# Performance work log

Hardware: AMD Instinct MI355X
Metric: run time of the kernel (lower is better)

The kernel has to match this reference:

```python
import jax, jax.numpy as jnp
import numpy as np

B, S, D = 1, 2048, 512
H, KH, DH = 8, 2, 64
G = H // KH            # grouped queries per kv head
CBS = SBS = 32         # compress / selection block size (equal)
NSEL = 8               # num selected blocks
WIN = 128              # sliding window size
NC = S // CBS          # num compressed blocks
NF = S // SBS          # num fine blocks (S divisible by SBS)
CDIM = CBS * DH


def setup_inputs():
    key = jax.random.key(0)
    ks = jax.random.split(key, 12)
    r = lambda k, shape, s=0.02: jax.random.normal(k, shape, dtype=jnp.float32) * s
    return {
        "inp": jax.random.normal(ks[0], (B, S, D), dtype=jnp.float32),
        "norm_w": jnp.ones((D,), jnp.float32),
        "w_qkv": r(ks[1], (D, H * DH + 2 * KH * DH)),
        "mem_kv": r(ks[2], (2, KH, 1, DH)),
        "k_pos": r(ks[3], (KH, CBS, DH)),
        "v_pos": r(ks[4], (KH, CBS, DH)),
        "kc_w1": r(ks[5], (CDIM, CDIM)), "kc_b1": jnp.zeros((CDIM,), jnp.float32),
        "kc_w2": r(ks[6], (CDIM, DH)), "kc_b2": jnp.zeros((DH,), jnp.float32),
        "vc_w1": r(ks[7], (CDIM, CDIM)), "vc_b1": jnp.zeros((CDIM,), jnp.float32),
        "vc_w2": r(ks[8], (CDIM, DH)), "vc_b2": jnp.zeros((DH,), jnp.float32),
        "comb_w": r(ks[9], (D, 3 * H)),
        "comb_b": jnp.tile(jnp.array([-2.0, -2.0, 2.0], jnp.float32), H),
        "out_w": r(ks[10], (H * DH, D)),
    }


def _rope(x):  # x: [b, h, n, d]; interleaved rotary (rotary-embedding-torch style)
    d, n = x.shape[-1], x.shape[-2]
    inv = 1.0 / (10000.0 ** (jnp.arange(0, d, 2, dtype=jnp.float32) / d))
    fr = jnp.arange(n, dtype=jnp.float32)[:, None] * inv[None, :]  # [n, d/2]
    fr = jnp.repeat(fr, 2, axis=-1)                                 # [n, d]
    cos, sin = jnp.cos(fr), jnp.sin(fr)
    xp = x.reshape(*x.shape[:-1], d // 2, 2)
    xr = jnp.stack((-xp[..., 1], xp[..., 0]), axis=-1).reshape(x.shape)
    return x * cos + xr * sin


def _mlp(x, w1, b1, w2, b2):
    return jax.nn.relu(x @ w1 + b1) @ w2 + b2


def _forward(inp, norm_w, w_qkv, mem_kv, k_pos, v_pos, kc_w1, kc_b1, kc_w2, kc_b2,
             vc_w1, vc_b1, vc_w2, vc_b2, comb_w, comb_b, out_w):
    scale = DH ** -0.5
    NEG = -jnp.finfo(jnp.float32).max

    # RMSNorm
    x = inp * jax.lax.rsqrt(jnp.mean(inp * inp, -1, keepdims=True)
                            + jnp.finfo(jnp.float32).eps) * norm_w

    qkv = x @ w_qkv
    q, k, v = jnp.split(qkv, [H * DH, H * DH + KH * DH], axis=-1)
    q = q.reshape(B, S, H, DH).transpose(0, 2, 1, 3)    # b h n d
    k = k.reshape(B, S, KH, DH).transpose(0, 2, 1, 3)   # b kh n d
    v = v.reshape(B, S, KH, DH).transpose(0, 2, 1, 3)

    # --- 1. compressed attention (unrotated q/k) ---
    kb = k.reshape(B, KH, NC, CBS, DH) + k_pos[None, :, None]
    vb = v.reshape(B, KH, NC, CBS, DH) + v_pos[None, :, None]
    ck = _mlp(kb.reshape(B, KH, NC, CDIM), kc_w1, kc_b1, kc_w2, kc_b2)  # b kh nc d
    cv = _mlp(vb.reshape(B, KH, NC, CDIM), vc_w1, vc_b1, vc_w2, vc_b2)
    ck = jnp.concatenate((jnp.broadcast_to(mem_kv[0][None], (B, KH, 1, DH)), ck), axis=2)
    cv = jnp.concatenate((jnp.broadcast_to(mem_kv[1][None], (B, KH, 1, DH)), cv), axis=2)

    ck_pos = jnp.concatenate((jnp.array([-1]), (jnp.arange(NC) + 1) * CBS - 1))
    cmask = ck_pos[None, :] < jnp.arange(S)[:, None]     # [S, 1+NC]

    qg = q.reshape(B, KH, G, S, DH)
    csim = jnp.einsum('bhgid,bhjd->bhgij', qg, ck) * scale
    csim = jnp.where(cmask, csim, NEG)
    cattn = jax.nn.softmax(csim, axis=-1)
    c_out = jnp.einsum('bhgij,bhjd->bhgid', cattn, cv)   # b kh g n d

    # --- importance scores -> top-k block selection (shared across grouped queries) ---
    imp = csim[..., 1:].mean(axis=2)                     # b kh n nc
    imp = jnp.pad(imp, ((0, 0), (0, 0), (0, 0), (1, 0)), constant_values=-1e3)
    imp = jax.nn.softmax(imp, axis=-1)[..., 1:]
    sel_val, sel_idx = jax.lax.top_k(imp, NSEL)          # b kh n sel

    # --- rotary for fine + sliding branches ---
    qr, kr = _rope(q), _rope(k)

    # --- 2. fine (selected-block) attention ---
    own = jnp.broadcast_to((jnp.arange(S) // SBS)[None, None, :, None], (B, KH, S, 1))
    sel_idx = jnp.concatenate((sel_idx, own), axis=-1)   # b kh n (sel+1), own block appended

    bmask = jnp.broadcast_to((sel_val > 1e-10)[..., None], (B, KH, S, NSEL, SBS))
    tri = jnp.tril(jnp.ones((SBS, SBS), bool))
    diag = jnp.broadcast_to(jnp.tile(tri, (NF, 1))[None, None, :, None, :], (B, KH, S, 1, SBS))
    fmask = jnp.concatenate((bmask, diag), axis=-2).reshape(B, KH, 1, S, (NSEL + 1) * SBS)

    kfb = kr.reshape(B, KH, NF, SBS, DH)
    vfb = v.reshape(B, KH, NF, SBS, DH)
    gidx = sel_idx[..., None, None]                      # b kh n sel1 1 1
    fk = jnp.take_along_axis(kfb[:, :, None], gidx, axis=3).reshape(B, KH, S, (NSEL + 1) * SBS, DH)
    fv = jnp.take_along_axis(vfb[:, :, None], gidx, axis=3).reshape(B, KH, S, (NSEL + 1) * SBS, DH)

    fqg = qr.reshape(B, KH, G, S, DH)
    fsim = jnp.einsum('bhgid,bhijd->bhgij', fqg, fk) * scale
    fsim = jnp.where(fmask, fsim, NEG)
    fattn = jax.nn.softmax(fsim, axis=-1)
    f_out = jnp.einsum('bhgij,bhijd->bhgid', fattn, fv)  # b kh g n d

    diff = jnp.arange(S)[:, None] - jnp.arange(S)[None, :]
    smask = (diff >= 0) & (diff <= WIN)
    ssim = jnp.einsum('bhgid,bhjd->bhgij', fqg, kr) * scale
    ssim = jnp.where(smask, ssim, NEG)
    sattn = jax.nn.softmax(ssim, axis=-1)
    s_out = jnp.einsum('bhgij,bhjd->bhgid', sattn, v)    # b kh g n d

    # --- learned gating combine over [compressed, fine, sliding] ---
    gates = jax.nn.sigmoid(x @ comb_w + comb_b).reshape(B, S, H, 3)
    gates = gates.transpose(0, 2, 1, 3).reshape(B, KH, G, S, 3)
    out = gates[..., 0:1] * c_out + gates[..., 1:2] * f_out + gates[..., 2:3] * s_out
    out = out.reshape(B, H, S, DH).transpose(0, 2, 1, 3).reshape(B, S, H * DH)
    return out @ out_w


def reference(inp, norm_w, w_qkv, mem_kv, k_pos, v_pos, kc_w1, kc_b1, kc_w2, kc_b2,
              vc_w1, vc_b1, vc_w2, vc_b2, comb_w, comb_b, out_w):
    return _forward(inp, norm_w, w_qkv, mem_kv, k_pos, v_pos, kc_w1, kc_b1, kc_w2, kc_b2,
                    vc_w1, vc_b1, vc_w2, vc_b2, comb_w, comb_b, out_w)
```

## Files before the change

### kernel.cpp

```cpp
#include <hip/hip_runtime.h>
#include <hip/hip_bf16.h>
#include <math.h>

#define S 2048
#define D 512
#define H 8
#define KH 2
#define DH 64
#define G 4
#define CBS 32
#define NSEL 8
#define WIN 128
#define NC 64
#define CDIM 2048

typedef __attribute__((ext_vector_type(8))) short bf16x8_t;
typedef __attribute__((ext_vector_type(4))) float f32x4_t;
typedef __attribute__((ext_vector_type(2))) _Float16 half2v;

static __device__ __forceinline__ unsigned short f2bf(float f) {
    union { float f; unsigned int u; } v; v.f = f;
    unsigned int r = (v.u + 0x7FFFu + ((v.u >> 16) & 1u)) >> 16;
    return (unsigned short)r;
}
static __device__ __forceinline__ float bf2f(unsigned short h) {
    union { unsigned int u; float f; } v; v.u = ((unsigned int)h) << 16;
    return v.f;
}
static __device__ __forceinline__ float bflo(unsigned int u) {
    union { unsigned int u; float f; } v; v.u = u << 16; return v.f;
}
static __device__ __forceinline__ float bfhi(unsigned int u) {
    union { unsigned int u; float f; } v; v.u = u & 0xffff0000u; return v.f;
}
static __device__ __forceinline__ unsigned short f2h(float f) {
    union { _Float16 h; unsigned short s; } v; v.h = (_Float16)f; return v.s;
}
static __device__ __forceinline__ float h2f(unsigned short u) {
    union { unsigned short s; _Float16 h; } v; v.s = u; return (float)v.h;
}
static __device__ __forceinline__ float dot2f16(unsigned int a, unsigned int b, float c) {
    union { unsigned int u; half2v h; } A, B; A.u = a; B.u = b;
    return __builtin_amdgcn_fdot2(A.h, B.h, c, false);
}

__global__ __launch_bounds__(256) void k_rmsnorm(const float* __restrict__ inp,
                                                 const float* __restrict__ w,
                                                 unsigned short* __restrict__ xbf) {
    int s = blockIdx.x; int t = threadIdx.x;
    const float* row = inp + (size_t)s * D;
    float a = row[t], b = row[t + 256];
    float ss = a * a + b * b;
    for (int off = 32; off; off >>= 1) ss += __shfl_xor(ss, off);
    __shared__ float red[4];
    if ((t & 63) == 0) red[t >> 6] = ss;
    __syncthreads();
    float tot = red[0] + red[1] + red[2] + red[3];
    float inv = rsqrtf(tot / (float)D + 1.1920929e-07f);
    xbf[(size_t)s * D + t]       = f2bf(a * inv * w[t]);
    xbf[(size_t)s * D + t + 256] = f2bf(b * inv * w[t + 256]);
}

__global__ void k_rope_table(float* __restrict__ ct, float* __restrict__ st) {
    int idx = blockIdx.x * 256 + threadIdx.x;
    int s = idx >> 5, p = idx & 31;
    float inv = powf(10000.0f, -(float)p / 32.0f);
    float fr = (float)s * inv;
    ct[idx] = cosf(fr); st[idx] = sinf(fr);
}

__global__ __launch_bounds__(256) void k_gemm0(
    const unsigned short* __restrict__ A,
    const float* __restrict__ W,
    const float* __restrict__ k_pos, const float* __restrict__ v_pos,
    const float* __restrict__ ct, const float* __restrict__ st,
    float* __restrict__ qb,
    unsigned short* __restrict__ qr16, unsigned short* __restrict__ kr16,
    unsigned short* __restrict__ v16, unsigned short* __restrict__ kbvb)
{
    const int K = 512, N = 768;
    __shared__ __align__(16) unsigned short As[64][40];
    __shared__ __align__(16) unsigned short Bs[64][40];
    int t = threadIdx.x;
    int m0 = blockIdx.y * 64, n0 = blockIdx.x * 64;
    int wave = t >> 6, lane = t & 63;
    int mh = wave & 1, nh = wave >> 1;
    f32x4_t acc[2][2] = {};
    int ar = t >> 2, ac = (t & 3) * 8;
    int bk = t >> 3, bn = (t & 7) * 8;
    int arow_l = lane & 15, kcol = (lane >> 4) * 8;
    uint4 aReg = *(const uint4*)&A[(size_t)(m0 + ar) * K + ac];
    const float4* wr = (const float4*)&W[(size_t)bk * N + n0 + bn];
    float4 w0 = wr[0], w1 = wr[1];
    for (int k0 = 0; k0 < K; k0 += 32) {
        __syncthreads();
        *(uint4*)&As[ar][ac] = aReg;
        unsigned short bp[8];
        bp[0] = f2bf(w0.x); bp[1] = f2bf(w0.y); bp[2] = f2bf(w0.z); bp[3] = f2bf(w0.w);
        bp[4] = f2bf(w1.x); bp[5] = f2bf(w1.y); bp[6] = f2bf(w1.z); bp[7] = f2bf(w1.w);
        #pragma unroll
        for (int j = 0; j < 8; ++j) Bs[bn + j][bk] = bp[j];
        __syncthreads();
        if (k0 + 32 < K) {
            aReg = *(const uint4*)&A[(size_t)(m0 + ar) * K + k0 + 32 + ac];
            wr = (const float4*)&W[(size_t)(k0 + 32 + bk) * N + n0 + bn];
            w0 = wr[0]; w1 = wr[1];
        }
        bf16x8_t a0 = *(const bf16x8_t*)&As[mh * 32 + arow_l][kcol];
        bf16x8_t a1 = *(const bf16x8_t*)&As[mh * 32 + 16 + arow_l][kcol];
        bf16x8_t b0v = *(const bf16x8_t*)&Bs[nh * 32 + arow_l][kcol];
        bf16x8_t b1v = *(const bf16x8_t*)&Bs[nh * 32 + 16 + arow_l][kcol];
        acc[0][0] = __builtin_amdgcn_mfma_f32_16x16x32_bf16(a0, b0v, acc[0][0], 0, 0, 0);
        acc[0][1] = __builtin_amdgcn_mfma_f32_16x16x32_bf16(a0, b1v, acc[0][1], 0, 0, 0);
        acc[1][0] = __builtin_amdgcn_mfma_f32_16x16x32_bf16(a1, b0v, acc[1][0], 0, 0, 0);
        acc[1][1] = __builtin_amdgcn_mfma_f32_16x16x32_bf16(a1, b1v, acc[1][1], 0, 0, 0);
    }
    #pragma unroll
    for (int mi = 0; mi < 2; ++mi)
    #pragma unroll
    for (int ni = 0; ni < 2; ++ni)
    #pragma unroll
    for (int r = 0; r < 4; ++r) {
        int gm = m0 + mh * 32 + mi * 16 + (lane >> 4) * 4 + r;
        int gn = n0 + nh * 32 + ni * 16 + (lane & 15);
        float val = acc[mi][ni][r];
        float part = __shfl_xor(val, 1);
        if (gn < 512) {
            int hh = gn >> 6, d = gn & 63;
            size_t idx = ((size_t)hh * S + gm) * DH + d;
            qb[idx] = val;
            int p = d >> 1;
            float cc = ct[gm * 32 + p], sn = st[gm * 32 + p];
            float y = (d & 1) ? (val * cc + part * sn) : (val * cc - part * sn);
            qr16[idx] = f2h(y);
        } else if (gn < 640) {
            int gk = gn - 512, khh = gk >> 6, d = gk & 63;
            size_t idx = ((size_t)khh * S + gm) * DH + d;
            int p = d >> 1;
            float cc = ct[gm * 32 + p], sn = st[gm * 32 + p];
            float y = (d & 1) ? (val * cc + part * sn) : (val * cc - part * sn);
            kr16[idx] = f2h(y);
            int tt = gm & 31, nc2 = gm >> 5;
            kbvb[((size_t)(khh * 64 + nc2)) * 2048 + tt * 64 + d] =
                f2bf(val + k_pos[(khh * CBS + tt) * 64 + d]);
        } else {
            int gv = gn - 640, khh = gv >> 6, d = gv & 63;
            size_t idx = ((size_t)khh * S + gm) * DH + d;
            v16[idx] = f2bf(val);
            int tt = gm & 31, nc2 = gm >> 5;
            kbvb[((size_t)(128 + khh * 64 + nc2)) * 2048 + tt * 64 + d] =
                f2bf(val + v_pos[(khh * CBS + tt) * 64 + d]);
        }
    }
}

template<int MODE>
__global__ __launch_bounds__(256) void k_gemm(
    const unsigned short* __restrict__ A,
    const float* __restrict__ B0,
    int M, int N, int K,
    float* __restrict__ outC)
{
    __shared__ __align__(16) unsigned short As[64][40];
    __shared__ __align__(16) unsigned short Bs[64][40];
    int t = threadIdx.x;
    int m0 = blockIdx.y * 64, n0 = blockIdx.x * 64;
    const float* W = B0;
    int wave = t >> 6, lane = t & 63;
    int mh = wave & 1, nh = wave >> 1;
    f32x4_t acc[2][2] = {};
    int ar = t >> 2, ac = (t & 3) * 8;
    int bk = t >> 3, bn = (t & 7) * 8;
    int arow_l = lane & 15, kcol = (lane >> 4) * 8;
    uint4 aReg = *(const uint4*)&A[(size_t)(m0 + ar) * K + ac];
    const float4* wr = (const float4*)&W[(size_t)bk * N + n0 + bn];
    float4 w0 = wr[0], w1 = wr[1];
    for (int k0 = 0; k0 < K; k0 += 32) {
        __syncthreads();
        *(uint4*)&As[ar][ac] = aReg;
        unsigned short bp[8];
        bp[0] = f2bf(w0.x); bp[1] = f2bf(w0.y); bp[2] = f2bf(w0.z); bp[3] = f2bf(w0.w);
        bp[4] = f2bf(w1.x); bp[5] = f2bf(w1.y); bp[6] = f2bf(w1.z); bp[7] = f2bf(w1.w);
        #pragma unroll
        for (int j = 0; j < 8; ++j) Bs[bn + j][bk] = bp[j];
        __syncthreads();
        if (k0 + 32 < K) {
            aReg = *(const uint4*)&A[(size_t)(m0 + ar) * K + k0 + 32 + ac];
            wr = (const float4*)&W[(size_t)(k0 + 32 + bk) * N + n0 + bn];
            w0 = wr[0]; w1 = wr[1];
        }
        bf16x8_t a0 = *(const bf16x8_t*)&As[mh * 32 + arow_l][kcol];
        bf16x8_t a1 = *(const bf16x8_t*)&As[mh * 32 + 16 + arow_l][kcol];
        bf16x8_t b0v = *(const bf16x8_t*)&Bs[nh * 32 + arow_l][kcol];
        bf16x8_t b1v = *(const bf16x8_t*)&Bs[nh * 32 + 16 + arow_l][kcol];
        acc[0][0] = __builtin_amdgcn_mfma_f32_16x16x32_bf16(a0, b0v, acc[0][0], 0, 0, 0);
        acc[0][1] = __builtin_amdgcn_mfma_f32_16x16x32_bf16(a0, b1v, acc[0][1], 0, 0, 0);
        acc[1][0] = __builtin_amdgcn_mfma_f32_16x16x32_bf16(a1, b0v, acc[1][0], 0, 0, 0);
        acc[1][1] = __builtin_amdgcn_mfma_f32_16x16x32_bf16(a1, b1v, acc[1][1], 0, 0, 0);
    }
    #pragma unroll
    for (int mi = 0; mi < 2; ++mi)
    #pragma unroll
    for (int ni = 0; ni < 2; ++ni)
    #pragma unroll
    for (int r = 0; r < 4; ++r) {
        int gm = m0 + mh * 32 + mi * 16 + (lane >> 4) * 4 + r;
        int gn = n0 + nh * 32 + ni * 16 + (lane & 15);
        outC[(size_t)gm * N + gn] = acc[mi][ni][r];
    }
}

__global__ __launch_bounds__(256) void k_gemm1p(
    const unsigned short* __restrict__ A,
    const float* __restrict__ kc_w1, const float* __restrict__ vc_w1,
    float* __restrict__ part)
{
    const int N = 2048, LDA = 2048;
    __shared__ __align__(16) unsigned short As[64][40];
    __shared__ __align__(16) unsigned short Bs[64][40];
    int t = threadIdx.x;
    int mb = blockIdx.y & 3, ks = blockIdx.y >> 2;
    int m0 = mb * 64, n0 = blockIdx.x * 64, kbeg = ks * 1024;
    const float* W = (mb >= 2) ? vc_w1 : kc_w1;
    int wave = t >> 6, lane = t & 63;
    int mh = wave & 1, nh = wave >> 1;
    f32x4_t acc[2][2] = {};
    int ar = t >> 2, ac = (t & 3) * 8;
    int bk = t >> 3, bn = (t & 7) * 8;
    int arow_l = lane & 15, kcol = (lane >> 4) * 8;
    uint4 aReg = *(const uint4*)&A[(size_t)(m0 + ar) * LDA + kbeg + ac];
    const float4* wr = (const float4*)&W[(size_t)(kbeg + bk) * N + n0 + bn];
    float4 w0 = wr[0], w1 = wr[1];
    for (int k0 = 0; k0 < 1024; k0 += 32) {
        __syncthreads();
        *(uint4*)&As[ar][ac] = aReg;
        unsigned short bp[8];
        bp[0] = f2bf(w0.x); bp[1] = f2bf(w0.y); bp[2] = f2bf(w0.z); bp[3] = f2bf(w0.w);
        bp[4] = f2bf(w1.x); bp[5] = f2bf(w1.y); bp[6] = f2bf(w1.z); bp[7] = f2bf(w1.w);
        #pragma unroll
        for (int j = 0; j < 8; ++j) Bs[bn + j][bk] = bp[j];
        __syncthreads();
        if (k0 + 32 < 1024) {
            aReg = *(const uint4*)&A[(size_t)(m0 + ar) * LDA + kbeg + k0 + 32 + ac];
            wr = (const float4*)&W[(size_t)(kbeg + k0 + 32 + bk) * N + n0 + bn];
            w0 = wr[0]; w1 = wr[1];
        }
        bf16x8_t a0 = *(const bf16x8_t*)&As[mh * 32 + arow_l][kcol];
        bf16x8_t a1 = *(const bf16x8_t*)&As[mh * 32 + 16 + arow_l][kcol];
        bf16x8_t b0v = *(const bf16x8_t*)&Bs[nh * 32 + arow_l][kcol];
        bf16x8_t b1v = *(const bf16x8_t*)&Bs[nh * 32 + 16 + arow_l][kcol];
        acc[0][0] = __builtin_amdgcn_mfma_f32_16x16x32_bf16(a0, b0v, acc[0][0], 0, 0, 0);
        acc[0][1] = __builtin_amdgcn_mfma_f32_16x16x32_bf16(a0, b1v, acc[0][1], 0, 0, 0);
        acc[1][0] = __builtin_amdgcn_mfma_f32_16x16x32_bf16(a1, b0v, acc[1][0], 0, 0, 0);
        acc[1][1] = __builtin_amdgcn_mfma_f32_16x16x32_bf16(a1, b1v, acc[1][1], 0, 0, 0);
    }
    #pragma unroll
    for (int mi = 0; mi < 2; ++mi)
    #pragma unroll
    for (int ni = 0; ni < 2; ++ni)
    #pragma unroll
    for (int r = 0; r < 4; ++r) {
        int gm = m0 + mh * 32 + mi * 16 + (lane >> 4) * 4 + r;
        int gn = n0 + nh * 32 + ni * 16 + (lane & 15);
        part[((size_t)ks * 256 + gm) * N + gn] = acc[mi][ni][r];
    }
}

__global__ __launch_bounds__(256) void k_gemm1r(
    const float4* __restrict__ part, const float* __restrict__ kc_b1,
    const float* __restrict__ vc_b1, uint2* __restrict__ hid)
{
    int idx = blockIdx.x * 256 + threadIdx.x;
    int gm = idx >> 9, gn4 = (idx & 511) * 4;
    float4 a = part[idx], b = part[idx + 131072];
    const float* bias = (gm >= 128) ? vc_b1 : kc_b1;
    float r0 = fmaxf(a.x + b.x + bias[gn4 + 0], 0.f);
    float r1 = fmaxf(a.y + b.y + bias[gn4 + 1], 0.f);
    float r2 = fmaxf(a.z + b.z + bias[gn4 + 2], 0.f);
    float r3 = fmaxf(a.w + b.w + bias[gn4 + 3], 0.f);
    uint2 o;
    o.x = (unsigned)f2bf(r0) | ((unsigned)f2bf(r1) << 16);
    o.y = (unsigned)f2bf(r2) | ((unsigned)f2bf(r3) << 16);
    hid[idx] = o;
}

__global__ __launch_bounds__(256) void k_mlp2p(
    const unsigned short* __restrict__ A,
    const float* __restrict__ kc_w2, const float* __restrict__ vc_w2,
    float* __restrict__ part)
{
    const int N = 64, LDA = 2048;
    __shared__ __align__(16) unsigned short As[64][40];
    __shared__ __align__(16) unsigned short Bs[64][40];
    int t = threadIdx.x;
    int ks = blockIdx.x, m0 = blockIdx.y * 64;
    int kbeg = ks * 512;
    const float* W = (blockIdx.y >= 2) ? vc_w2 : kc_w2;
    int wave = t >> 6, lane = t & 63;
    int mh = wave & 1, nh = wave >> 1;
    f32x4_t acc[2][2] = {};
    int ar = t >> 2, ac = (t & 3) * 8;
    int bk = t >> 3, bn = (t & 7) * 8;
    int arow_l = lane & 15, kcol = (lane >> 4) * 8;
    uint4 aReg = *(const uint4*)&A[(size_t)(m0 + ar) * LDA + kbeg + ac];
    const float4* wr = (const float4*)&W[(size_t)(kbeg + bk) * N + bn];
    float4 w0 = wr[0], w1 = wr[1];
    for (int k0 = 0; k0 < 512; k0 += 32) {
        __syncthreads();
        *(uint4*)&As[ar][ac] = aReg;
        unsigned short bp[8];
        bp[0] = f2bf(w0.x); bp[1] = f2bf(w0.y); bp[2] = f2bf(w0.z); bp[3] = f2bf(w0.w);
        bp[4] = f2bf(w1.x); bp[5] = f2bf(w1.y); bp[6] = f2bf(w1.z); bp[7] = f2bf(w1.w);
        #pragma unroll
        for (int j = 0; j < 8; ++j) Bs[bn + j][bk] = bp[j];
        __syncthreads();
        if (k0 + 32 < 512) {
            aReg = *(const uint4*)&A[(size_t)(m0 + ar) * LDA + kbeg + k0 + 32 + ac];
            wr = (const float4*)&W[(size_t)(kbeg + k0 + 32 + bk) * N + bn];
            w0 = wr[0]; w1 = wr[1];
        }
        bf16x8_t a0 = *(const bf16x8_t*)&As[mh * 32 + arow_l][kcol];
        bf16x8_t a1 = *(const bf16x8_t*)&As[mh * 32 + 16 + arow_l][kcol];
        bf16x8_t b0v = *(const bf16x8_t*)&Bs[nh * 32 + arow_l][kcol];
        bf16x8_t b1v = *(const bf16x8_t*)&Bs[nh * 32 + 16 + arow_l][kcol];
        acc[0][0] = __builtin_amdgcn_mfma_f32_16x16x32_bf16(a0, b0v, acc[0][0], 0, 0, 0);
        acc[0][1] = __builtin_amdgcn_mfma_f32_16x16x32_bf16(a0, b1v, acc[0][1], 0, 0, 0);
        acc[1][0] = __builtin_amdgcn_mfma_f32_16x16x32_bf16(a1, b0v, acc[1][0], 0, 0, 0);
        acc[1][1] = __builtin_amdgcn_mfma_f32_16x16x32_bf16(a1, b1v, acc[1][1], 0, 0, 0);
    }
    #pragma unroll
    for (int mi = 0; mi < 2; ++mi)
    #pragma unroll
    for (int ni = 0; ni < 2; ++ni)
    #pragma unroll
    for (int r = 0; r < 4; ++r) {
        int gm = m0 + mh * 32 + mi * 16 + (lane >> 4) * 4 + r;
        int gn = nh * 32 + ni * 16 + (lane & 15);
        part[((size_t)ks * 256 + gm) * 64 + gn] = acc[mi][ni][r];
    }
}

__global__ __launch_bounds__(256) void k_mlp2r(
    const float* __restrict__ part, const float* __restrict__ kc_b2,
    const float* __restrict__ vc_b2, const float* __restrict__ mem_kv,
    float* __restrict__ ck, float* __restrict__ cv)
{
    int idx = blockIdx.x * 256 + threadIdx.x;
    int gm = idx >> 6, gn = idx & 63;
    float sum = part[(size_t)gm * 64 + gn] + part[(size_t)(256 + gm) * 64 + gn]
              + part[(size_t)(512 + gm) * 64 + gn] + part[(size_t)(768 + gm) * 64 + gn];
    bool isv = gm >= 128;
    sum += isv ? vc_b2[gn] : kc_b2[gn];
    float* dst = isv ? cv : ck;
    int kh2 = (gm >> 6) & 1, nc2 = gm & 63;
    dst[(kh2 * 65 + 1 + nc2) * 64 + gn] = sum;
    if (blockIdx.x == 0 && threadIdx.x < 256) {
        int t = threadIdx.x;
        int path2 = t >> 7, khm = (t >> 6) & 1, dm = t & 63;
        float* dstm = path2 ? cv : ck;
        dstm[khm * 65 * 64 + dm] = mem_kv[path2 * (KH * DH) + khm * DH + dm];
    }
}

__global__ __launch_bounds__(256) void k_cattn(
    const float* __restrict__ q, const float* __restrict__ ck, const float* __restrict__ cv,
    float* __restrict__ c_out, int* __restrict__ sel)
{
    int kh = blockIdx.x >> 9, sc = blockIdx.x & 511;
    int s_base = sc * 4;
    __shared__ float ckT[64][65];
    __shared__ float cvL[64][66];
    __shared__ float qL[4][64];
    __shared__ float simL[4][64];
    __shared__ float pL[4][64];
    int t = threadIdx.x;
    for (int idx = t; idx < 4096; idx += 256) {
        int j = idx >> 6, d = idx & 63;
        ckT[d][j] = ck[(kh * 65 + j) * 64 + d];
        cvL[j][d] = cv[(kh * 65 + j) * 64 + d];
    }
    int g = t >> 6, lane = t & 63;
    for (int si = 0; si < 4; ++si) {
        int s = s_base + si;
        __syncthreads();
        qL[g][lane] = q[((kh * G + g) * S + s) * DH + lane];
        __syncthreads();
        int j = lane;
        bool valid = (j == 0) || (s >= j * 32);
        float sim = 0.f;
        #pragma unroll 8
        for (int d = 0; d < 64; ++d) sim += qL[g][d] * ckT[d][j];
        sim *= 0.125f;
        float simm = valid ? sim : -INFINITY;
        simL[g][j] = simm;
        float m = simm;
        for (int off = 32; off; off >>= 1) m = fmaxf(m, __shfl_xor(m, off));
        float p = valid ? __expf(simm - m) : 0.f;
        float den = p;
        for (int off = 32; off; off >>= 1) den += __shfl_xor(den, off);
        pL[g][j] = p / den;
        float acc = 0.f;
        #pragma unroll
        for (int j4 = 0; j4 < 16; ++j4) {
            float4 p4 = *(const float4*)&pL[g][j4 * 4];
            acc += p4.x * cvL[j4 * 4 + 0][lane] + p4.y * cvL[j4 * 4 + 1][lane]
                 + p4.z * cvL[j4 * 4 + 2][lane] + p4.w * cvL[j4 * 4 + 3][lane];
        }
        c_out[((kh * G + g) * S + s) * DH + lane] = acc;
        __syncthreads();
        if (g == 0) {
            int l = lane;
            float lv = -INFINITY;
            if (l < 63 && s >= (l + 1) * 32)
                lv = 0.25f * (simL[0][l + 1] + simL[1][l + 1] + simL[2][l + 1] + simL[3][l + 1]);
            float mm = lv;
            for (int off = 32; off; off >>= 1) mm = fmaxf(mm, __shfl_xor(mm, off));
            mm = fmaxf(mm, -1000.0f);
            float e = (lv == -INFINITY) ? 0.f : __expf(lv - mm);
            float dd = e;
            for (int off = 32; off; off >>= 1) dd += __shfl_xor(dd, off);
            dd += __expf(-1000.0f - mm);
            float val = e / dd;
            float vc = val;
            int base = (kh * S + s) * 9;
            for (int t8 = 0; t8 < 8; ++t8) {
                float bv2 = vc; int bi = l;
                for (int off = 32; off; off >>= 1) {
                    float ov = __shfl_xor(bv2, off); int oi = __shfl_xor(bi, off);
                    if (ov > bv2 || (ov == bv2 && oi < bi)) { bv2 = ov; bi = oi; }
                }
                if (l == 0) sel[base + t8] = (bv2 > 1e-10f) ? bi : -1;
                if (l == bi) vc = -1.f;
            }
            if (l == 0) sel[base + 8] = s >> 5;
        }
    }
}

__global__ __launch_bounds__(256, 4) void k_swattn(
    const unsigned short* __restrict__ qr16, const unsigned short* __restrict__ kr16,
    const unsigned short* __restrict__ v16, const int* __restrict__ sel,
    float* __restrict__ fob, float* __restrict__ sob)
{
    int kh = blockIdx.x >> 11, s = blockIdx.x & 2047;
    int t = threadIdx.x, w = t >> 6, lane = t & 63, g = w;
    __shared__ __align__(16) unsigned char KL[64 * 128];
    __shared__ __align__(16) unsigned char VL[64 * 144];
    __shared__ unsigned short qL16[4][64];
    __shared__ float pL[4][64];

    qL16[g][lane] = qr16[(((size_t)kh * G + g) * S + s) * DH + lane];

    int base = (kh * S + s) * 9;
    int lo = s - WIN; if (lo < 0) lo = 0;

    int nv = 0;
    #pragma unroll
    for (int i = 0; i < 8; ++i) nv += (sel[base + i] >= 0) ? 1 : 0;
    int npairF = (nv + 1) >> 1;
    int nchS = (s - lo + 63) >> 6;
    int nch = npairF + nchS;
    int ownStart = s & ~31;
    bool hasOwn = (s & 31) != 0;

    float lF = 0.f, lS = 0.f;
    float a0F = 0.f, a1F = 0.f, a0S = 0.f, a1S = 0.f;
    int h = lane >> 5, dhalf = lane & 31;
    int key = w * 16 + (lane & 15);
    int grpA = lane >> 4;
    uint4 z = make_uint4(0, 0, 0, 0);
    uint4 kd0 = z, kd1 = z, vd0 = z, vd1 = z;

    auto issue = [&](int c) {
        int gkey; bool kv;
        if (c < npairF) {
            int b = sel[base + 2 * c + ((key >> 5) & 1)];
            kv = b >= 0;
            gkey = (kv ? b : 0) * 32 + (key & 31);
        } else {
            gkey = lo + (c - npairF) * 64 + key;
            kv = gkey < s;
        }
        const uint4* kp = (const uint4*)&kr16[((size_t)kh * S + gkey) * DH];
        const uint4* vp = (const uint4*)&v16 [((size_t)kh * S + gkey) * DH];
        kd0 = kv ? kp[grpA] : z;
        kd1 = kv ? kp[grpA + 4] : z;
        vd0 = kv ? vp[grpA] : z;
        vd1 = kv ? vp[grpA + 4] : z;
    };

    issue(0);
    for (int c = 0; c < nch; ++c) {
        __syncthreads();
        *(uint4*)(KL + key * 128 + 16 * (grpA ^ (key & 7))) = kd0;
        *(uint4*)(KL + key * 128 + 16 * ((grpA + 4) ^ (key & 7))) = kd1;
        *(uint4*)(VL + key * 144 + 16 * grpA) = vd0;
        *(uint4*)(VL + key * 144 + 16 * (grpA + 4)) = vd1;
        __syncthreads();
        if (c + 1 < nch) issue(c + 1);

        int j = lane;
        bool isPair = c < npairF;
        int cs = c - npairF;
        int gk0 = lo + cs * 64;
        bool valid = isPair ? ((j < 32) || ((2 * c + 1) < nv))
                            : ((gk0 + j) < s);

        float sva = 0.f, svb = 0.f, svc = 0.f, svd = 0.f;
        #pragma unroll
        for (int grp = 0; grp < 8; ++grp) {
            uint4 kk = *(const uint4*)(KL + j * 128 + 16 * (grp ^ (j & 7)));
            uint4 qq = *(const uint4*)((const unsigned char*)qL16 + g * 128 + 16 * grp);
            sva = dot2f16(kk.x, qq.x, sva);
            svb = dot2f16(kk.y, qq.y, svb);
            svc = dot2f16(kk.z, qq.z, svc);
            svd = dot2f16(kk.w, qq.w, svd);
        }
        float sv = (sva + svb) + (svc + svd);
        float p = valid ? __expf(sv * 0.125f) : 0.f;
        pL[g][j] = p;

        bool doOwn = (!isPair) && hasOwn && (cs == nchS - 1);
        if (!doOwn) {
            if (isPair) lF += p; else lS += p;
            float t0 = 0.f, t1 = 0.f;
            #pragma unroll
            for (int j4 = 0; j4 < 8; ++j4) {
                float4 p4 = *(const float4*)&pL[g][h * 32 + j4 * 4];
                const float* pp = (const float*)&p4;
                #pragma unroll
                for (int q2 = 0; q2 < 4; ++q2) {
                    unsigned int v2 = *(const unsigned int*)(VL + (h * 32 + j4 * 4 + q2) * 144 + 4 * dhalf);
                    t0 += pp[q2] * bflo(v2);
                    t1 += pp[q2] * bfhi(v2);
                }
            }
            if (isPair) { a0F += t0; a1F += t1; }
            else        { a0S += t0; a1S += t1; }
        } else {
            lS += p;
            int jstart = ownStart - gk0;
            if (j >= jstart) lF += p;
            float pre0 = 0.f, pre1 = 0.f, suf0 = 0.f, suf1 = 0.f;
            #pragma unroll
            for (int j4 = 0; j4 < 8; ++j4) {
                float4 p4 = *(const float4*)&pL[g][h * 32 + j4 * 4];
                const float* pp = (const float*)&p4;
                #pragma unroll
                for (int q2 = 0; q2 < 4; ++q2) {
                    int jj = h * 32 + j4 * 4 + q2;
                    unsigned int v2 = *(const unsigned int*)(VL + jj * 144 + 4 * dhalf);
                    float t0 = pp[q2] * bflo(v2);
                    float t1 = pp[q2] * bfhi(v2);
                    bool inSuf = jj >= jstart;
                    suf0 += inSuf ? t0 : 0.f;
                    suf1 += inSuf ? t1 : 0.f;
                    pre0 += inSuf ? 0.f : t0;
                    pre1 += inSuf ? 0.f : t1;
                }
            }
            a0S += pre0 + suf0; a1S += pre1 + suf1;
            a0F += suf0;        a1F += suf1;
        }
    }
    {
        float pr = h2f(qL16[g][lane]) * h2f(kr16[((size_t)kh * S + s) * DH + lane]);
        for (int off = 32; off; off >>= 1) pr += __shfl_xor(pr, off);
        float pd = __expf(pr * 0.125f);
        for (int off = 32; off; off >>= 1) {
            lF += __shfl_xor(lF, off);
            lS += __shfl_xor(lS, off);
        }
        lF += pd; lS += pd;
        if (h == 0) {
            unsigned int v2 = *(const unsigned int*)&v16[(((size_t)kh * S + s) * DH) + 2 * dhalf];
            float b0 = bflo(v2), b1 = bfhi(v2);
            a0F += pd * b0; a1F += pd * b1;
            a0S += pd * b0; a1S += pd * b1;
        }
    }
    a0F += __shfl_xor(a0F, 32);
    a1F += __shfl_xor(a1F, 32);
    a0S += __shfl_xor(a0S, 32);
    a1S += __shfl_xor(a1S, 32);
    if (lane < 32) {
        size_t ob = (((size_t)kh * G + g) * S + s) * DH + 2 * dhalf;
        float invF = 1.f / lF, invS = 1.f / lS;
        *(float2*)&fob[ob] = make_float2(a0F * invF, a1F * invF);
        *(float2*)&sob[ob] = make_float2(a0S * invS, a1S * invS);
    }
}

__global__ __launch_bounds__(256) void k_combine(
    const unsigned short* __restrict__ xbf, const float* __restrict__ comb_w, const float* __restrict__ comb_b,
    const float* __restrict__ c_out, const float* __restrict__ f_out, const float* __restrict__ s_out,
    unsigned short* __restrict__ comb)
{
    int s = blockIdx.x, t = threadIdx.x;
    __shared__ float gpart[24][8];
    __shared__ float gates[24];
    if (t < 192) {
        int cc = t >> 3, pt = t & 7;
        float sum = 0.f;
        for (int d = pt * 64; d < pt * 64 + 64; ++d)
            sum += bf2f(xbf[s * D + d]) * comb_w[d * 24 + cc];
        gpart[cc][pt] = sum;
    }
    __syncthreads();
    if (t < 24) {
        float sum = comb_b[t];
        for (int i = 0; i < 8; ++i) sum += gpart[t][i];
        gates[t] = 1.f / (1.f + __expf(-sum));
    }
    __syncthreads();
    for (int o = t; o < 512; o += 256) {
        int h = o >> 6, d = o & 63;
        int idx = (h * S + s) * DH + d;
        float r = gates[h * 3] * c_out[idx] + gates[h * 3 + 1] * f_out[idx] + gates[h * 3 + 2] * s_out[idx];
        comb[s * D + o] = f2bf(r);
    }
}

extern "C" void kernel_launch(void* const* d_in, const int* in_sizes, int n_in,
                              void* d_out, int out_size, void* d_ws, size_t ws_size,
                              hipStream_t stream)
{
    (void)in_sizes; (void)n_in; (void)out_size; (void)ws_size;
    const float* inp    = (const float*)d_in[0];
    const float* norm_w = (const float*)d_in[1];
    const float* w_qkv  = (const float*)d_in[2];
    const float* mem_kv = (const float*)d_in[3];
    const float* k_pos  = (const float*)d_in[4];
    const float* v_pos  = (const float*)d_in[5];
    const float* kc_w1  = (const float*)d_in[6];
    const float* kc_b1  = (const float*)d_in[7];
    const float* kc_w2  = (const float*)d_in[8];
    const float* kc_b2  = (const float*)d_in[9];
    const float* vc_w1  = (const float*)d_in[10];
    const float* vc_b1  = (const float*)d_in[11];
    const float* vc_w2  = (const float*)d_in[12];
    const float* vc_b2  = (const float*)d_in[13];
    const float* comb_w = (const float*)d_in[14];
    const float* comb_b = (const float*)d_in[15];
    const float* out_w  = (const float*)d_in[16];
    float* out = (float*)d_out;

    char* w = (char*)d_ws;
    size_t off = 0;
    auto alloc = [&](size_t bytes) { void* p = w + off; off += (bytes + 255) & ~(size_t)255; return p; };
    unsigned short* xbf   = (unsigned short*)alloc((size_t)S * D * 2);
    unsigned short* kbvb  = (unsigned short*)alloc((size_t)256 * 2048 * 2);
    unsigned short* hid   = (unsigned short*)alloc((size_t)256 * 2048 * 2);
    unsigned short* combb = (unsigned short*)alloc((size_t)S * 512 * 2);
    unsigned short* qr16  = (unsigned short*)alloc((size_t)H * S * DH * 2);
    unsigned short* kr16  = (unsigned short*)alloc((size_t)KH * S * DH * 2);
    unsigned short* v16   = (unsigned short*)alloc((size_t)KH * S * DH * 2);
    float* qb   = (float*)alloc((size_t)H * S * DH * 4);
    float* ckb  = (float*)alloc((size_t)KH * 65 * 64 * 4);
    float* cvb  = (float*)alloc((size_t)KH * 65 * 64 * 4);
    float* cob  = (float*)alloc((size_t)H * S * DH * 4);
    float* fob  = (float*)alloc((size_t)H * S * DH * 4);
    float* sob  = (float*)alloc((size_t)H * S * DH * 4);
    float* ctab = (float*)alloc((size_t)S * 32 * 4);
    float* stab = (float*)alloc((size_t)S * 32 * 4);
    float* partb = (float*)alloc((size_t)4 * 256 * 64 * 4);
    float* g1part = (float*)alloc((size_t)2 * 256 * 2048 * 4);
    int*   selb = (int*)alloc((size_t)KH * S * 9 * 4);

    k_rope_table<<<(S * 32) / 256, 256, 0, stream>>>(ctab, stab);

    k_rmsnorm<<<S, 256, 0, stream>>>(inp, norm_w, xbf);

    k_gemm0<<<dim3(768 / 64, S / 64), 256, 0, stream>>>(
        xbf, w_qkv, k_pos, v_pos, ctab, stab, qb, qr16, kr16, v16, kbvb);

    k_gemm1p<<<dim3(32, 8), 256, 0, stream>>>(kbvb, kc_w1, vc_w1, g1part);
    k_gemm1r<<<512, 256, 0, stream>>>((const float4*)g1part, kc_b1, vc_b1, (uint2*)hid);

    k_mlp2p<<<dim3(4, 4), 256, 0, stream>>>(hid, kc_w2, vc_w2, partb);
    k_mlp2r<<<64, 256, 0, stream>>>(partb, kc_b2, vc_b2, mem_kv, ckb, cvb);

    k_cattn<<<KH * 512, 256, 0, stream>>>(qb, ckb, cvb, cob, selb);

    k_swattn<<<KH * S, 256, 0, stream>>>(qr16, kr16, v16, selb, fob, sob);

    k_combine<<<S, 256, 0, stream>>>(xbf, comb_w, comb_b, cob, fob, sob, combb);
    k_gemm<2><<<dim3(512 / 64, S / 64), 256, 0, stream>>>(
        combb, out_w, S, 512, 512, out);
}
```

Measured before the change: 220.2 us.

## Process 128-key chunks in sliding/selected attention with split K/V loading

The chunk size in the fused selected and sliding-window attention kernel is doubled from 64 to 128 keys. Selected blocks are now processed four at a time, and the whole window fits in a single chunk, which halves the number of loop iterations and barrier pairs. Loading is reorganised so half the threads fetch a full K row and the other half a full V row, with eight 16-byte prefetch registers per thread. The cost is double the shared memory and more registers, which may reduce occupancy under launch_bounds(256,4), plus wasted work on invalid keys when few blocks are selected.

```diff
diff --git a/kernel.cpp b/kernel.cpp
--- a/kernel.cpp
+++ b/kernel.cpp
@@ -444,10 +444,10 @@
 {
     int kh = blockIdx.x >> 11, s = blockIdx.x & 2047;
     int t = threadIdx.x, w = t >> 6, lane = t & 63, g = w;
-    __shared__ __align__(16) unsigned char KL[64 * 128];
-    __shared__ __align__(16) unsigned char VL[64 * 144];
+    __shared__ __align__(16) unsigned char KL[128 * 128];
+    __shared__ __align__(16) unsigned char VL[128 * 144];
     __shared__ unsigned short qL16[4][64];
-    __shared__ float pL[4][64];
+    __shared__ float pL[4][128];
 
     qL16[g][lane] = qr16[(((size_t)kh * G + g) * S + s) * DH + lane];
 
@@ -457,98 +457,122 @@
     int nv = 0;
     #pragma unroll
     for (int i = 0; i < 8; ++i) nv += (sel[base + i] >= 0) ? 1 : 0;
-    int npairF = (nv + 1) >> 1;
-    int nchS = (s - lo + 63) >> 6;
-    int nch = npairF + nchS;
+    int nquadF = (nv + 3) >> 2;
+    int nchS = (s > 0) ? 1 : 0;
+    int nch = nquadF + nchS;
     int ownStart = s & ~31;
     bool hasOwn = (s & 31) != 0;
+    int jstart = ownStart - lo;
 
     float lF = 0.f, lS = 0.f;
     float a0F = 0.f, a1F = 0.f, a0S = 0.f, a1S = 0.f;
     int h = lane >> 5, dhalf = lane & 31;
-    int key = w * 16 + (lane & 15);
-    int grpA = lane >> 4;
+    int skey = t & 127;
+    bool isV = t >= 128;
+    const unsigned short* srcbuf = isV ? v16 : kr16;
     uint4 z = make_uint4(0, 0, 0, 0);
-    uint4 kd0 = z, kd1 = z, vd0 = z, vd1 = z;
+    uint4 pf0 = z, pf1 = z, pf2 = z, pf3 = z, pf4 = z, pf5 = z, pf6 = z, pf7 = z;
 
     auto issue = [&](int c) {
         int gkey; bool kv;
-        if (c < npairF) {
-            int b = sel[base + 2 * c + ((key >> 5) & 1)];
+        if (c < nquadF) {
+            int b = sel[base + 4 * c + (skey >> 5)];
             kv = b >= 0;
-            gkey = (kv ? b : 0) * 32 + (key & 31);
+            gkey = (kv ? b : 0) * 32 + (skey & 31);
         } else {
-            gkey = lo + (c - npairF) * 64 + key;
+            gkey = lo + skey;
             kv = gkey < s;
         }
-        const uint4* kp = (const uint4*)&kr16[((size_t)kh * S + gkey) * DH];
-        const uint4* vp = (const uint4*)&v16 [((size_t)kh * S + gkey) * DH];
-        kd0 = kv ? kp[grpA] : z;
-        kd1 = kv ? kp[grpA + 4] : z;
-        vd0 = kv ? vp[grpA] : z;
-        vd1 = kv ? vp[grpA + 4] : z;
+        const uint4* sp = (const uint4*)&srcbuf[((size_t)kh * S + gkey) * DH];
+        pf0 = kv ? sp[0] : z; pf1 = kv ? sp[1] : z;
+        pf2 = kv ? sp[2] : z; pf3 = kv ? sp[3] : z;
+        pf4 = kv ? sp[4] : z; pf5 = kv ? sp[5] : z;
+        pf6 = kv ? sp[6] : z; pf7 = kv ? sp[7] : z;
     };
 
     issue(0);
     for (int c = 0; c < nch; ++c) {
         __syncthreads();
-        *(uint4*)(KL + key * 128 + 16 * (grpA ^ (key & 7))) = kd0;
-        *(uint4*)(KL + key * 128 + 16 * ((grpA + 4) ^ (key & 7))) = kd1;
-        *(uint4*)(VL + key * 144 + 16 * grpA) = vd0;
-        *(uint4*)(VL + key * 144 + 16 * (grpA + 4)) = vd1;
+        if (!isV) {
+            int sb = skey & 7;
+            *(uint4*)(KL + skey * 128 + 16 * (0 ^ sb)) = pf0;
+            *(uint4*)(KL + skey * 128 + 16 * (1 ^ sb)) = pf1;
+            *(uint4*)(KL + skey * 128 + 16 * (2 ^ sb)) = pf2;
+            *(uint4*)(KL + skey * 128 + 16 * (3 ^ sb)) = pf3;
+            *(uint4*)(KL + skey * 128 + 16 * (4 ^ sb)) = pf4;
+            *(uint4*)(KL + skey * 128 + 16 * (5 ^ sb)) = pf5;
+            *(uint4*)(KL + skey * 128 + 16 * (6 ^ sb)) = pf6;
+            *(uint4*)(KL + skey * 128 + 16 * (7 ^ sb)) = pf7;
+        } else {
+            *(uint4*)(VL + skey * 144 +   0) = pf0;
+            *(uint4*)(VL + skey * 144 +  16) = pf1;
+            *(uint4*)(VL + skey * 144 +  32) = pf2;
+            *(uint4*)(VL + skey * 144 +  48) = pf3;
+            *(uint4*)(VL + skey * 144 +  64) = pf4;
+            *(uint4*)(VL + skey * 144 +  80) = pf5;
+            *(uint4*)(VL + skey * 144 +  96) = pf6;
+            *(uint4*)(VL + skey * 144 + 112) = pf7;
+        }
         __syncthreads();
         if (c + 1 < nch) issue(c + 1);
 
         int j = lane;
-        bool isPair = c < npairF;
-        int cs = c - npairF;
-        int gk0 = lo + cs * 64;
-        bool valid = isPair ? ((j < 32) || ((2 * c + 1) < nv))
-                            : ((gk0 + j) < s);
-
-        float sva = 0.f, svb = 0.f, svc = 0.f, svd = 0.f;
+        bool isQuad = c < nquadF;
+        bool valid0, valid1;
+        if (isQuad) {
+            valid0 = (4 * c + (j >> 5)) < nv;
+            valid1 = (4 * c + 2 + (j >> 5)) < nv;
+        } else {
+            valid0 = (lo + j) < s;
+            valid1 = (lo + 64 + j) < s;
+        }
+
+        float s0a = 0.f, s0b = 0.f, s0c = 0.f, s0d = 0.f;
+        float s1a = 0.f, s1b = 0.f, s1c = 0.f, s1d = 0.f;
         #pragma unroll
         for (int grp = 0; grp < 8; ++grp) {
-            uint4 kk = *(const uint4*)(KL + j * 128 + 16 * (grp ^ (j & 7)));
             uint4 qq = *(const uint4*)((const unsigned char*)qL16 + g * 128 + 16 * grp);
-            sva = dot2f16(kk.x, qq.x, sva);
-            svb = dot2f16(kk.y, qq.y, svb);
-            svc = dot2f16(kk.z, qq.z, svc);
-            svd = dot2f16(kk.w, qq.w, svd);
-        }
-        float sv = (sva + svb) + (svc + svd);
-        float p = valid ? __expf(sv * 0.125f) : 0.f;
-        pL[g][j] = p;
-
-        bool doOwn = (!isPair) && hasOwn && (cs == nchS - 1);
+            int swz = 16 * (grp ^ (j & 7));
+            uint4 k0 = *(const uint4*)(KL + j * 128 + swz);
+            uint4 k1 = *(const uint4*)(KL + (j + 64) * 128 + swz);
+            s0a = dot2f16(k0.x, qq.x, s0a); s0b = dot2f16(k0.y, qq.y, s0b);
+            s0c = dot2f16(k0.z, qq.z, s0c); s0d = dot2f16(k0.w, qq.w, s0d);
+            s1a = dot2f16(k1.x, qq.x, s1a); s1b = dot2f16(k1.y, qq.y, s1b);
+            s1c = dot2f16(k1.z, qq.z, s1c); s1d = dot2f16(k1.w, qq.w, s1d);
+        }
+        float p0 = valid0 ? __expf(((s0a + s0b) + (s0c + s0d)) * 0.125f) : 0.f;
+        float p1 = valid1 ? __expf(((s1a + s1b) + (s1c + s1d)) * 0.125f) : 0.f;
+        pL[g][j] = p0;
+        pL[g][j + 64] = p1;
+
+        bool doOwn = (!isQuad) && hasOwn;
         if (!doOwn) {
-            if (isPair) lF += p; else lS += p;
             float t0 = 0.f, t1 = 0.f;
             #pragma unroll
-            for (int j4 = 0; j4 < 8; ++j4) {
-                float4 p4 = *(const float4*)&pL[g][h * 32 + j4 * 4];
+            for (int j4 = 0; j4 < 16; ++j4) {
+                float4 p4 = *(const float4*)&pL[g][h * 64 + j4 * 4];
                 const float* pp = (const float*)&p4;
                 #pragma unroll
                 for (int q2 = 0; q2 < 4; ++q2) {
-                    unsigned int v2 = *(const unsigned int*)(VL + (h * 32 + j4 * 4 + q2) * 144 + 4 * dhalf);
+                    unsigned int v2 = *(const unsigned int*)(VL + (h * 64 + j4 * 4 + q2) * 144 + 4 * dhalf);
                     t0 += pp[q2] * bflo(v2);
                     t1 += pp[q2] * bfhi(v2);
                 }
             }
-            if (isPair) { a0F += t0; a1F += t1; }
-            else        { a0S += t0; a1S += t1; }
+            if (isQuad) { a0F += t0; a1F += t1; lF += p0 + p1; }
+            else        { a0S += t0; a1S += t1; lS += p0 + p1; }
         } else {
-            lS += p;
-            int jstart = ownStart - gk0;
-            if (j >= jstart) lF += p;
+            lS += p0 + p1;
+            if (j >= jstart) lF += p0;
+            if (j + 64 >= jstart) lF += p1;
             float pre0 = 0.f, pre1 = 0.f, suf0 = 0.f, suf1 = 0.f;
             #pragma unroll
-            for (int j4 = 0; j4 < 8; ++j4) {
-                float4 p4 = *(const float4*)&pL[g][h * 32 + j4 * 4];
+            for (int j4 = 0; j4 < 16; ++j4) {
+                float4 p4 = *(const float4*)&pL[g][h * 64 + j4 * 4];
                 const float* pp = (const float*)&p4;
                 #pragma unroll
                 for (int q2 = 0; q2 < 4; ++q2) {
-                    int jj = h * 32 + j4 * 4 + q2;
+                    int jj = h * 64 + j4 * 4 + q2;
                     unsigned int v2 = *(const unsigned int*)(VL + jj * 144 + 4 * dhalf);
                     float t0 = pp[q2] * bflo(v2);
                     float t1 = pp[q2] * bfhi(v2);
```

Measured after the change: 226.5 us. +2.9%, slower.
